# Kernel optimization log

Hardware: AMD Instinct MI355X
Metric: run time of the kernel (lower is better)

Reference implementation:

```python
import jax, jax.numpy as jnp
import numpy as np

B, S, D, H = 2, 2048, 1024, 16
DK = D // H


def setup_inputs() -> dict:
    key = jax.random.key(0)
    ks = jax.random.split(key, 9)
    scale = 1.0 / np.sqrt(D)
    inp = {
        "x": jax.random.normal(ks[0], (B, S, D), dtype=jnp.float32),
        "mask": jnp.triu(jnp.ones((S, S), dtype=jnp.int32), k=1),  # 1 = masked (causal)
        "Wq": jax.random.normal(ks[1], (D, D), dtype=jnp.float32) * scale,
        "bq": jnp.zeros((D,), dtype=jnp.float32),
        "Wk": jax.random.normal(ks[2], (D, D), dtype=jnp.float32) * scale,
        "bk": jnp.zeros((D,), dtype=jnp.float32),
        "Wv": jax.random.normal(ks[3], (D, D), dtype=jnp.float32) * scale,
        "bv": jnp.zeros((D,), dtype=jnp.float32),
        "Wo": jax.random.normal(ks[4], (D, D), dtype=jnp.float32) * scale,
        "bo": jnp.zeros((D,), dtype=jnp.float32),
    }
    return inp


def reference(x, mask, Wq, bq, Wk, bk, Wv, bv, Wo, bo):
    # Linear projections (torch nn.Linear: x @ W.T + b; here W stored as (D, D) in
    # (in, out) layout so x @ W + b is equivalent math).
    q = x @ Wq + bq  # (B, S, D)
    k = x @ Wk + bk
    v = x @ Wv + bv
    # Split heads: (B, S, D) -> (B, H, S, DK)
    def split(t):
        return t.reshape(B, S, H, DK).transpose(0, 2, 1, 3)
    q, k, v = split(q), split(k), split(v)
    # Scaled dot-product attention with full score matrix (faithful to original)
    scores = jnp.einsum("bhsd,bhtd->bhst", q, k) / jnp.sqrt(jnp.float32(DK))
    scores = jnp.where(mask[None, None, :, :] == 1, -jnp.inf, scores)
    attn = jax.nn.softmax(scores, axis=-1)  # (B, H, S, S)
    out = jnp.einsum("bhst,bhtd->bhsd", attn, v)
    # Merge heads and final projection
    out = out.transpose(0, 2, 1, 3).reshape(B, S, D)
    return out @ Wo + bo
```

## Files before the change

### kernel.cpp

```cpp
#include <hip/hip_runtime.h>
#include <hip/hip_bf16.h>
#include <cstdint>
#include <cstddef>

typedef __attribute__((ext_vector_type(8))) short short8;
typedef __attribute__((ext_vector_type(4))) float f32x4;
typedef __attribute__((ext_vector_type(4))) unsigned int u32x4;
typedef unsigned short u16;
typedef unsigned int u32;

#define NB 2
#define NS 2048
#define ND 1024
#define NH 16
#define NDK 64

__device__ __forceinline__ u16 f2bf(float f){
  u32 u = __builtin_bit_cast(u32, f);
  u += 0x7fffu + ((u >> 16) & 1u);
  return (u16)(u >> 16);
}

__device__ __forceinline__ u32 pk2(float lo, float hi){
  return (u32)f2bf(lo) | ((u32)f2bf(hi) << 16);
}

__device__ __forceinline__ u32 cvtpk(float lo, float hi){
  u32 r;
  asm("v_cvt_pk_bf16_f32 %0, %1, %2" : "=v"(r) : "v"(lo), "v"(hi));
  return r;
}

__device__ __forceinline__ float fexp2(float x){
  float r;
  asm("v_exp_f32 %0, %1" : "=v"(r) : "v"(x));
  return r;
}

__device__ __forceinline__ void stage16(const u16* g, u16* l, int lane){
#if defined(__has_builtin) && __has_builtin(__builtin_amdgcn_global_load_lds)
  __builtin_amdgcn_global_load_lds(
      (const __attribute__((address_space(1))) u32*)(const void*)g,
      (__attribute__((address_space(3))) u32*)(void*)l, 16, 0, 0);
#else
  ((uint4*)l)[lane] = *(const uint4*)g;
#endif
}


__global__ __launch_bounds__(256) void prep_kernel(
    const float* __restrict__ Wq, const float* __restrict__ Wk,
    const float* __restrict__ Wv, const float* __restrict__ Wo,
    const float* __restrict__ x,
    u16* __restrict__ Wt, u16* __restrict__ xb)
{
  const int z = blockIdx.z;
  const int tx = threadIdx.x, ty = threadIdx.y;
  if (z == 4){
    const int base = ((blockIdx.y*32 + (int)blockIdx.x)*256 + ty*32 + tx)*16;
    float4 v0 = *(const float4*)(x+base);
    float4 v1 = *(const float4*)(x+base+4);
    float4 v2 = *(const float4*)(x+base+8);
    float4 v3 = *(const float4*)(x+base+12);
    const int blk = base & ~31;
    const int h4  = (base & 16) ? 4 : 0;
    *(uint2*)(xb + blk +  0 + h4) = make_uint2(pk2(v0.x,v0.y), pk2(v0.z,v0.w));
    *(uint2*)(xb + blk +  8 + h4) = make_uint2(pk2(v1.x,v1.y), pk2(v1.z,v1.w));
    *(uint2*)(xb + blk + 16 + h4) = make_uint2(pk2(v2.x,v2.y), pk2(v2.z,v2.w));
    *(uint2*)(xb + blk + 24 + h4) = make_uint2(pk2(v3.x,v3.y), pk2(v3.z,v3.w));
    return;
  }
  const float* W = (z==0)?Wq:(z==1)?Wk:(z==2)?Wv:Wo;
  u16* dst = Wt + (size_t)z*ND*ND;
  __shared__ float t[32][33];
  const int n0 = blockIdx.x*32, k0 = blockIdx.y*32;
  const int ptx = 8*((tx&15)>>2) + (tx&3) + 4*(tx>>4);
#pragma unroll
  for (int i=0;i<4;i++) t[ty+i*8][tx] = W[(size_t)(k0+ty+i*8)*ND + n0+tx];
  __syncthreads();
#pragma unroll
  for (int i=0;i<4;i++) dst[(size_t)(n0+ty+i*8)*ND + k0+ptx] = f2bf(t[tx][ty+i*8]);
}

template<int MODE>
__global__ __launch_bounds__(256,3) void gemm_kernel(
    const u16* __restrict__ Abf, const u16* __restrict__ Wtz,
    const float* __restrict__ bias0, const float* __restrict__ bias1, const float* __restrict__ bias2,
    u16* __restrict__ Qout, u16* __restrict__ Kout, u16* __restrict__ Vtout,
    float* __restrict__ Fout)
{
  constexpr int MI = (MODE==0) ? 4 : 2;
  constexpr int AROWS = MI*32;
  int bx, by;
  if constexpr (MODE==0){
    const int f  = blockIdx.x;
    const int fp = (f & 7)*96 + (f >> 3);
    by = fp / 24; bx = fp % 24;
  } else { bx = blockIdx.x; by = blockIdx.y; }
  const int tid  = threadIdx.x;
  const int lane = tid & 63;
  const int wv   = tid >> 6;
  const int a = lane & 15, g = lane >> 4;
  const int wm = wv >> 1, wn = wv & 1;
  const int m0 = by * AROWS, n0 = bx * 128;
  const int z  = (MODE==0) ? (n0 >> 10) : 0;

  __shared__ u16 Al[AROWS*64];
  __shared__ u16 Bl[128*64];

  f32x4 acc[MI][4] = {};

  const int grow = lane >> 3;
  const int gcol = (lane & 7) * 8;

#pragma unroll 1
  for (int k0 = 0; k0 < ND; k0 += 64) {
    __syncthreads();
#pragma unroll
    for (int i=0;i<MI;++i){
      const int r = (AROWS/4)*wv + 8*i + grow;
      const int cs = gcol ^ ((r&7)<<3);
      stage16(Abf + (size_t)(m0+r)*ND + k0 + cs, &Al[((AROWS/4)*wv+8*i)*64], lane);
    }
#pragma unroll
    for (int i=0;i<4;++i){
      const int r = 32*wv + 8*i + grow;
      const int cs = gcol ^ ((r&7)<<3);
      stage16(Wtz + (size_t)(n0+r)*ND + k0 + cs, &Bl[(32*wv+8*i)*64], lane);
    }
    __syncthreads();

#pragma unroll
    for (int kk=0; kk<64; kk+=32){
      short8 af[MI], bfr[4];
#pragma unroll
      for (int mi=0;mi<MI;++mi){
        const int rr = wm*(MI*16) + mi*16 + a;
        const int rsw = (rr&7)<<3;
        af[mi] = *(const short8*)(&Al[rr*64] + ((kk + 8*g) ^ rsw));
      }
#pragma unroll
      for (int ni=0;ni<4;++ni){
        const int rr = wn*64 + ni*16 + a;
        const int rsw = (rr&7)<<3;
        bfr[ni] = *(const short8*)(&Bl[rr*64] + ((kk + 8*g) ^ rsw));
      }
      __builtin_amdgcn_s_setprio(1);
#pragma unroll
      for (int mi=0;mi<MI;++mi)
#pragma unroll
        for (int ni=0;ni<4;++ni)
          acc[mi][ni] = __builtin_amdgcn_mfma_f32_16x16x32_bf16(af[mi], bfr[ni], acc[mi][ni], 0,0,0);
      __builtin_amdgcn_s_setprio(0);
    }
  }

#pragma unroll
  for (int mi=0;mi<MI;++mi){
#pragma unroll
    for (int ni=0;ni<4;++ni){
      const int n  = n0 + wn*64 + ni*16 + a;
      const int mb = m0 + wm*(MI*16) + mi*16 + 4*g;
      if constexpr (MODE==0){
        const int nn = n & 1023;
        const float* bp = (z==0)? bias0 : (z==1)? bias1 : bias2;
        const float bias = bp[nn];
        const int h = nn >> 6, dk = nn & 63;
        const int b = mb >> 11, s = mb & 2047;
        if (z==2){
          const int sb = s & 31;
          const int col = (s & ~31) + 8*((sb&15)>>2) + 4*(sb>>4);
          *(uint2*)&Vtout[(((size_t)b*NH + h)*NDK + dk)*NS + col] =
            make_uint2(pk2(acc[mi][ni][0]+bias, acc[mi][ni][1]+bias),
                       pk2(acc[mi][ni][2]+bias, acc[mi][ni][3]+bias));
        } else {
          u16* dst = (z==0)? Qout : Kout;
          const float sc = (z==0)? 0.1803368801111601f : 1.0f;
          const int d5 = dk & 31;
          const int pdk = (dk & 32) + 8*((d5&15)>>2) + (d5&3) + 4*(d5>>4);
#pragma unroll
          for (int r=0;r<4;++r)
            dst[(((size_t)b*NH + h)*NS + (s+r))*NDK + pdk] = f2bf((acc[mi][ni][r]+bias)*sc);
        }
      } else {
        const float bias = bias0[n];
#pragma unroll
        for (int r=0;r<4;++r)
          Fout[(size_t)(mb+r)*ND + n] = acc[mi][ni][r] + bias;
      }
    }
  }
}

#define KOFF(p_, q_) ((p_)*8192 + (q_)*4096)
#define VOFF(p_, q_) (16384 + (p_)*8192 + (q_)*4096)
#define FIXM 10.0f

__global__ __launch_bounds__(512,4) void attn_kernel(
    const u16* __restrict__ Qg, const u16* __restrict__ Kg,
    const u16* __restrict__ Vtg, u16* __restrict__ Og)
{
  const int tid  = threadIdx.x;
  const int lane = tid & 63, wv = tid >> 6;
  const int qw = wv & 3, par = wv >> 2;
  const int a = lane & 15, g = lane >> 4;
  const int bh = blockIdx.x;
  const int qt = blockIdx.y;
  const int qb = (qt < 8) ? qt : (23 - qt);
  const int qB  = qb * 128;
  const int q0w = qB + qw*32;
  const int nr  = qb + 1;

  __shared__ u16 SH[32768];

  short8 qf[2][2];
#pragma unroll
  for (int qi=0; qi<2; ++qi){
    const u16* qptr = Qg + ((size_t)bh*NS + q0w + qi*16 + a)*NDK;
    qf[qi][0] = *(const short8*)(qptr + 8*g);
    qf[qi][1] = *(const short8*)(qptr + 32 + 8*g);
  }

  const short8 ones8 = {(short)0x3F80,(short)0x3F80,(short)0x3F80,(short)0x3F80,
                        (short)0x3F80,(short)0x3F80,(short)0x3F80,(short)0x3F80};
  f32x4 lacc[2] = {};
  f32x4 accO[4][2] = {};

  const int srow = wv*8 + (lane >> 3);
  const int scol = (lane & 7) * 8;
  const int scs  = scol ^ ((srow & 7) << 3);
  const u16* kgp = Kg  + (size_t)bh*NS*NDK + (size_t)srow*NDK + scs;
  const u16* vgp = Vtg + (size_t)bh*NDK*NS + (size_t)srow*NS  + scs;

  stage16(kgp,            &SH[KOFF(0,0) + wv*512], lane);
  stage16(kgp + 64*NDK,   &SH[KOFF(0,1) + wv*512], lane);
  stage16(vgp,            &SH[VOFF(0,0) + wv*512], lane);
  stage16(vgp + 64,       &SH[VOFF(0,1) + wv*512], lane);
  __syncthreads();

  const u16* kstg = kgp + 128*NDK;
  const u16* vstg = vgp + 128;

  int cur = 0;
#pragma unroll 1
  for (int r=0; r<nr; ++r){
    const int t = 2*r + par;
    const int kv0 = t * 64;
    if (r+1 < nr){
      stage16(kstg,          &SH[KOFF(cur^1,0) + wv*512], lane);
      stage16(kstg + 64*NDK, &SH[KOFF(cur^1,1) + wv*512], lane);
      stage16(vstg,          &SH[VOFF(cur^1,0) + wv*512], lane);
      stage16(vstg + 64,     &SH[VOFF(cur^1,1) + wv*512], lane);
      kstg += 128*NDK; vstg += 128;
    }

    if (kv0 <= q0w + 31){
      const u16* Kb = &SH[KOFF(cur,par)];
      const u16* Vb = &SH[VOFF(cur,par)];
      f32x4 sc[2][4];
#pragma unroll
      for (int qi=0; qi<2; ++qi)
#pragma unroll
        for (int kvf=0; kvf<4; ++kvf)
          sc[qi][kvf] = (f32x4){-FIXM, -FIXM, -FIXM, -FIXM};
      __builtin_amdgcn_s_setprio(1);
#pragma unroll
      for (int kvf=0; kvf<4; ++kvf){
        const int rr = kvf*16 + a;
        const int rsw = (rr&7)<<3;
        const u16* rp = Kb + rr*64;
        short8 kf0 = *(const short8*)(rp + ((8*g) ^ rsw));
        short8 kf1 = *(const short8*)(rp + ((32 + 8*g) ^ rsw));
#pragma unroll
        for (int qi=0; qi<2; ++qi){
          sc[qi][kvf] = __builtin_amdgcn_mfma_f32_16x16x32_bf16(kf0, qf[qi][0], sc[qi][kvf], 0,0,0);
          sc[qi][kvf] = __builtin_amdgcn_mfma_f32_16x16x32_bf16(kf1, qf[qi][1], sc[qi][kvf], 0,0,0);
        }
      }
      __builtin_amdgcn_s_setprio(0);

      const bool dm = (kv0 + 63 > q0w);
      short8 pf[2][2];
#pragma unroll
      for (int qi=0; qi<2; ++qi){
        const int q = q0w + qi*16 + a;
        if (dm){
#pragma unroll
          for (int kvf=0;kvf<4;++kvf)
#pragma unroll
            for (int rr=0;rr<4;++rr){
              const int kv = kv0 + kvf*16 + 4*g + rr;
              if (kv > q) sc[qi][kvf][rr] = -1e30f;
            }
        }
        u32 pw[2][4];
#pragma unroll
        for (int kvf=0;kvf<4;++kvf){
          const float e0 = fexp2(sc[qi][kvf][0]);
          const float e1 = fexp2(sc[qi][kvf][1]);
          const float e2 = fexp2(sc[qi][kvf][2]);
          const float e3 = fexp2(sc[qi][kvf][3]);
          pw[kvf>>1][(kvf&1)*2+0] = cvtpk(e0,e1);
          pw[kvf>>1][(kvf&1)*2+1] = cvtpk(e2,e3);
        }
        pf[qi][0] = __builtin_bit_cast(short8, *(u32x4*)pw[0]);
        pf[qi][1] = __builtin_bit_cast(short8, *(u32x4*)pw[1]);
      }

      __builtin_amdgcn_s_setprio(1);
#pragma unroll
      for (int qi=0; qi<2; ++qi){
        lacc[qi] = __builtin_amdgcn_mfma_f32_16x16x32_bf16(ones8, pf[qi][0], lacc[qi], 0,0,0);
        lacc[qi] = __builtin_amdgcn_mfma_f32_16x16x32_bf16(ones8, pf[qi][1], lacc[qi], 0,0,0);
      }
#pragma unroll
      for (int dkg=0;dkg<4;++dkg){
        const int rr = dkg*16 + a;
        const int rsw = (rr&7)<<3;
        const u16* rp = Vb + rr*64;
        short8 vf0 = *(const short8*)(rp + ((8*g) ^ rsw));
        short8 vf1 = *(const short8*)(rp + ((32 + 8*g) ^ rsw));
#pragma unroll
        for (int qi=0; qi<2; ++qi){
          accO[dkg][qi] = __builtin_amdgcn_mfma_f32_16x16x32_bf16(vf0, pf[qi][0], accO[dkg][qi], 0,0,0);
          accO[dkg][qi] = __builtin_amdgcn_mfma_f32_16x16x32_bf16(vf1, pf[qi][1], accO[dkg][qi], 0,0,0);
        }
      }
      __builtin_amdgcn_s_setprio(0);
    }

    __syncthreads();
    cur ^= 1;
  }

  float* ms = (float*)SH;
  if (par == 1){
#pragma unroll
    for (int qi=0; qi<2; ++qi){
      const int idx = (((qw*64 + lane)*2) + qi)*17;
#pragma unroll
      for (int dkg=0;dkg<4;++dkg)
#pragma unroll
        for (int j=0;j<4;++j) ms[idx + dkg*4 + j] = accO[dkg][qi][j];
      ms[idx+16] = lacc[qi][0];
    }
  }
  __syncthreads();

  if (par == 0){
    u16* Lw = &SH[18432] + qw*2048;
#pragma unroll
    for (int qi=0; qi<2; ++qi){
      const int idx = (((qw*64 + lane)*2) + qi)*17;
      const float linv = 1.0f / (lacc[qi][0] + ms[idx+16]);
      const int row = qi*16 + a;
#pragma unroll
      for (int dkg=0; dkg<4; ++dkg){
        const int pcol = 32*(dkg>>1) + 8*g + 4*(dkg&1);
        const float o0 = (accO[dkg][qi][0] + ms[idx+dkg*4+0])*linv;
        const float o1 = (accO[dkg][qi][1] + ms[idx+dkg*4+1])*linv;
        const float o2 = (accO[dkg][qi][2] + ms[idx+dkg*4+2])*linv;
        const float o3 = (accO[dkg][qi][3] + ms[idx+dkg*4+3])*linv;
        *(uint2*)&Lw[(row<<6) + (pcol ^ ((row&7)<<3))] = make_uint2(cvtpk(o0,o1), cvtpk(o2,o3));
      }
    }
    const int b = bh >> 4, h = bh & 15;
#pragma unroll
    for (int j=0; j<4; ++j){
      const int row = j*8 + (lane>>3);
      const int cc  = (lane&7)*8;
      uint4 d = *(const uint4*)&Lw[(row<<6) + (cc ^ ((row&7)<<3))];
      *(uint4*)(Og + ((size_t)b*NS + qB + qw*32 + row)*ND + h*NDK + cc) = d;
    }
  }
}

extern "C" void kernel_launch(void* const* d_in, const int* in_sizes, int n_in,
                              void* d_out, int out_size, void* d_ws, size_t ws_size,
                              hipStream_t stream) {
  (void)in_sizes; (void)n_in; (void)out_size; (void)ws_size;
  const float* x  = (const float*)d_in[0];
  const float* Wq = (const float*)d_in[2];
  const float* bq = (const float*)d_in[3];
  const float* Wk = (const float*)d_in[4];
  const float* bk = (const float*)d_in[5];
  const float* Wv = (const float*)d_in[6];
  const float* bv = (const float*)d_in[7];
  const float* Wo = (const float*)d_in[8];
  const float* bo = (const float*)d_in[9];
  float* out = (float*)d_out;

  u16* Wt  = (u16*)d_ws;
  u16* Qb  = Wt  + (size_t)4194304;
  u16* Kb  = Qb  + (size_t)4194304;
  u16* Vtb = Kb  + (size_t)4194304;
  u16* XO  = Vtb + (size_t)4194304;

  prep_kernel<<<dim3(32,32,5), dim3(32,8,1), 0, stream>>>(Wq, Wk, Wv, Wo, x, Wt, XO);
  gemm_kernel<0><<<dim3(768), dim3(256), 0, stream>>>(
      XO, Wt, bq, bk, bv, Qb, Kb, Vtb, (float*)nullptr);
  attn_kernel<<<dim3(32,16), dim3(512), 0, stream>>>(Qb, Kb, Vtb, XO);
  gemm_kernel<1><<<dim3(8,64), dim3(256), 0, stream>>>(
      XO, Wt + (size_t)3*1048576, bo, nullptr, nullptr,
      (u16*)nullptr, (u16*)nullptr, (u16*)nullptr, out);
}
```

Before: 91.01 us.

## Load K/V fragments directly from global memory instead of LDS double-buffering

Removes the shared-memory double-buffered staging of K and V tiles and the per-iteration block barrier. Each wave now reads its MFMA K and V fragments straight from global memory (relying on L1/L2 caching), advancing the pointers each round. This drops the LDS traffic and synchronisation but loses the explicit prefetch and cooperative reuse across the four waves sharing a tile, so the loop becomes exposed to global-load latency and repeated L2 reads.

Result: slower. 128.6 us (+41.3%).

```diff
diff --git a/kernel.cpp b/kernel.cpp
--- a/kernel.cpp
+++ b/kernel.cpp
@@ -192,8 +192,6 @@
   }
 }
 
-#define KOFF(p_, q_) ((p_)*8192 + (q_)*4096)
-#define VOFF(p_, q_) (16384 + (p_)*8192 + (q_)*4096)
 #define FIXM 10.0f
 
 __global__ __launch_bounds__(512,4) void attn_kernel(
@@ -226,37 +224,18 @@
   f32x4 lacc[2] = {};
   f32x4 accO[4][2] = {};
 
-  const int srow = wv*8 + (lane >> 3);
-  const int scol = (lane & 7) * 8;
-  const int scs  = scol ^ ((srow & 7) << 3);
-  const u16* kgp = Kg  + (size_t)bh*NS*NDK + (size_t)srow*NDK + scs;
-  const u16* vgp = Vtg + (size_t)bh*NDK*NS + (size_t)srow*NS  + scs;
-
-  stage16(kgp,            &SH[KOFF(0,0) + wv*512], lane);
-  stage16(kgp + 64*NDK,   &SH[KOFF(0,1) + wv*512], lane);
-  stage16(vgp,            &SH[VOFF(0,0) + wv*512], lane);
-  stage16(vgp + 64,       &SH[VOFF(0,1) + wv*512], lane);
-  __syncthreads();
-
-  const u16* kstg = kgp + 128*NDK;
-  const u16* vstg = vgp + 128;
-
-  int cur = 0;
+  const u16* kp = Kg + ((size_t)bh*NS + (size_t)par*64 + a)*NDK + 8*g;
+  const u16* vp0 = Vtg + ((size_t)bh*NDK +  0 + a)*NS + par*64 + 8*g;
+  const u16* vp1 = Vtg + ((size_t)bh*NDK + 16 + a)*NS + par*64 + 8*g;
+  const u16* vp2 = Vtg + ((size_t)bh*NDK + 32 + a)*NS + par*64 + 8*g;
+  const u16* vp3 = Vtg + ((size_t)bh*NDK + 48 + a)*NS + par*64 + 8*g;
+
 #pragma unroll 1
   for (int r=0; r<nr; ++r){
     const int t = 2*r + par;
     const int kv0 = t * 64;
-    if (r+1 < nr){
-      stage16(kstg,          &SH[KOFF(cur^1,0) + wv*512], lane);
-      stage16(kstg + 64*NDK, &SH[KOFF(cur^1,1) + wv*512], lane);
-      stage16(vstg,          &SH[VOFF(cur^1,0) + wv*512], lane);
-      stage16(vstg + 64,     &SH[VOFF(cur^1,1) + wv*512], lane);
-      kstg += 128*NDK; vstg += 128;
-    }
 
     if (kv0 <= q0w + 31){
-      const u16* Kb = &SH[KOFF(cur,par)];
-      const u16* Vb = &SH[VOFF(cur,par)];
       f32x4 sc[2][4];
 #pragma unroll
       for (int qi=0; qi<2; ++qi)
@@ -266,11 +245,8 @@
       __builtin_amdgcn_s_setprio(1);
 #pragma unroll
       for (int kvf=0; kvf<4; ++kvf){
-        const int rr = kvf*16 + a;
-        const int rsw = (rr&7)<<3;
-        const u16* rp = Kb + rr*64;
-        short8 kf0 = *(const short8*)(rp + ((8*g) ^ rsw));
-        short8 kf1 = *(const short8*)(rp + ((32 + 8*g) ^ rsw));
+        short8 kf0 = *(const short8*)(kp + kvf*1024);
+        short8 kf1 = *(const short8*)(kp + kvf*1024 + 32);
 #pragma unroll
         for (int qi=0; qi<2; ++qi){
           sc[qi][kvf] = __builtin_amdgcn_mfma_f32_16x16x32_bf16(kf0, qf[qi][0], sc[qi][kvf], 0,0,0);
@@ -315,11 +291,9 @@
       }
 #pragma unroll
       for (int dkg=0;dkg<4;++dkg){
-        const int rr = dkg*16 + a;
-        const int rsw = (rr&7)<<3;
-        const u16* rp = Vb + rr*64;
-        short8 vf0 = *(const short8*)(rp + ((8*g) ^ rsw));
-        short8 vf1 = *(const short8*)(rp + ((32 + 8*g) ^ rsw));
+        const u16* rp = (dkg==0)? vp0 : (dkg==1)? vp1 : (dkg==2)? vp2 : vp3;
+        short8 vf0 = *(const short8*)(rp);
+        short8 vf1 = *(const short8*)(rp + 32);
 #pragma unroll
         for (int qi=0; qi<2; ++qi){
           accO[dkg][qi] = __builtin_amdgcn_mfma_f32_16x16x32_bf16(vf0, pf[qi][0], accO[dkg][qi], 0,0,0);
@@ -329,8 +303,8 @@
       __builtin_amdgcn_s_setprio(0);
     }
 
-    __syncthreads();
-    cur ^= 1;
+    kp  += 8192;
+    vp0 += 128; vp1 += 128; vp2 += 128; vp3 += 128;
   }
 
   float* ms = (float*)SH;
```
